# Kernel optimization log

Measured on AMD Instinct MI355X. Metric: run time of the kernel, lower is better.

The kernel has to match this reference:

```python
import jax, jax.numpy as jnp
import numpy as np

NUM_HEADS = 16
SLICE_SIZE = 1024
SCALING = SLICE_SIZE ** 0.5  # module divides by sqrt(slice_size), as written


def setup_inputs() -> dict:
    key = jax.random.key(0)
    ks = jax.random.split(key, 9)
    B, S, D = 4, 2048, SLICE_SIZE
    sc = 0.02
    return {
        "x": jax.random.normal(ks[0], (B, S, D), dtype=jnp.float32),
        "Wq": jax.random.normal(ks[1], (D, D), dtype=jnp.float32) * sc,
        "bq": jax.random.normal(ks[2], (D,), dtype=jnp.float32) * sc,
        "Wk": jax.random.normal(ks[3], (D, D), dtype=jnp.float32) * sc,
        "bk": jax.random.normal(ks[4], (D,), dtype=jnp.float32) * sc,
        "Wv": jax.random.normal(ks[5], (D, D), dtype=jnp.float32) * sc,
        "bv": jax.random.normal(ks[6], (D,), dtype=jnp.float32) * sc,
        "Wp": jax.random.normal(ks[7], (D, D), dtype=jnp.float32) * sc,
        "bp": jax.random.normal(ks[8], (D,), dtype=jnp.float32) * sc,
    }


def _split_heads(t):
    # 'b s (h o) -> b h s o'
    b, s, d = t.shape
    return t.reshape(b, s, NUM_HEADS, d // NUM_HEADS).transpose(0, 2, 1, 3)


def reference(x, Wq, bq, Wk, bk, Wv, bv, Wp, bp):
    q = _split_heads(x @ Wq.T + bq)  # [B,H,S,O]
    k = _split_heads(x @ Wk.T + bk)
    v = _split_heads(x @ Wv.T + bv)
    energy = jnp.einsum('bhqo,bhko->bhqk', q, k)  # full score matrix
    attn = jax.nn.softmax(energy / SCALING, axis=-1)
    # Faithful to source: 'b h q k, b h v o -> b h v o' sums attn over (q,k)
    out = jnp.einsum('bhqk,bhvo->bhvo', attn, v)
    b, h, s, o = out.shape
    out = out.transpose(0, 2, 1, 3).reshape(b, s, h * o)  # 'b h v o -> b v (h o)'
    return out @ Wp.T + bp
```

## Files before the change

kernel.cpp:

```cpp
#include <hip/hip_runtime.h>
#include <cstdint>


typedef unsigned short u16;
typedef __bf16 bf16x8 __attribute__((ext_vector_type(8)));
typedef unsigned short u16x8 __attribute__((ext_vector_type(8)));
typedef float f32x4 __attribute__((ext_vector_type(4)));

__device__ __forceinline__ u16 f2bf(float f) {
  unsigned int u = __float_as_uint(f);
  u += 0x7fffu + ((u >> 16) & 1u);
  return (u16)(u >> 16);
}

__device__ __forceinline__ void load16(const void* g, void* l) {
  auto gp = (const __attribute__((address_space(1))) unsigned int*)(uintptr_t)g;
  auto lp = (__attribute__((address_space(3))) unsigned int*)(unsigned int)(uintptr_t)l;
  __builtin_amdgcn_global_load_lds(gp, lp, 16, 0, 0);
}

__global__ void k_prep(const float* __restrict__ Wv, const float* __restrict__ bv,
                       const float* __restrict__ Wp, const float* __restrict__ bp,
                       u16* __restrict__ wvtb, float* __restrict__ cv) {
  __shared__ float tile[32][33];
  const int b = blockIdx.x;
  const int tid = threadIdx.x;
  if (b < 1024) {
    const int bi = (b & 31) * 32;
    const int bj = (b >> 5) * 32;
    const int tx = tid & 31;
    const int ty = tid >> 5;
    for (int r = ty; r < 32; r += 8)
      tile[r][tx] = Wv[(long)(bj + r) * 1024 + bi + tx];
    __syncthreads();
    for (int r = ty; r < 32; r += 8)
      wvtb[(long)(bi + r) * 1024 + bj + tx] = f2bf(tile[tx][r]);
  } else {
    const int row = (b - 1024) * 4 + (tid >> 6);
    const int lane = tid & 63;
    const float* w = Wp + (long)row * 1024;
    float s = 0.f;
    for (int j = lane; j < 1024; j += 64) s += w[j] * bv[j];
    for (int off = 32; off; off >>= 1) s += __shfl_down(s, off, 64);
    if (lane == 0) cv[row] = 2048.f * s + bp[row];
  }
}

__global__ void k_reduce(const float* __restrict__ p, u16* __restrict__ dst) {
  const long i = (long)(blockIdx.x * 256 + threadIdx.x) * 4;
  const float4 a = *(const float4*)(p + i);
  const float4 b = *(const float4*)(p + 1048576 + i);
  const float4 c = *(const float4*)(p + 2097152 + i);
  const float4 d = *(const float4*)(p + 3145728 + i);
  ushort4 o;
  o.x = f2bf((a.x + b.x + c.x + d.x) * 2048.f);
  o.y = f2bf((a.y + b.y + c.y + d.y) * 2048.f);
  o.z = f2bf((a.z + b.z + c.z + d.z) * 2048.f);
  o.w = f2bf((a.w + b.w + c.w + d.w) * 2048.f);
  *(ushort4*)(dst + i) = o;
}

template <int MODE, int NB>
__global__ __launch_bounds__(256, 3) void k_gemm(
    const float* __restrict__ A, const u16* __restrict__ B, float* __restrict__ Out,
    const float* __restrict__ bias, int M, int N, int K) {
  __shared__ u16 As[64 * 64];
  __shared__ u16 Bs[256 * 64];

  const int tid = threadIdx.x;
  const int lane = tid & 63;
  const int wv = tid >> 6;
  const int waveN = wv << 6;
  const int l15 = lane & 15;
  const int quad = lane >> 4;

  long bm, bn;
  int kBeg, kEnd;
  if constexpr (MODE == 0) {
    const int id = blockIdx.x;
    const int xcd = id & 7;
    const int j = id >> 3;
    const int mPerXcd = M / 64 / 8;
    bm = (long)(xcd * mPerXcd + j / NB) * 64;
    bn = (long)(j % NB) * 256;
    kBeg = 0; kEnd = K;
  } else {
    bm = (long)blockIdx.x * 64;
    bn = (long)blockIdx.y * 256;
    const int kChunk = K / gridDim.z;
    kBeg = blockIdx.z * kChunk;
    kEnd = kBeg + kChunk;
  }

  const int ar = tid >> 2;
  const int acg = tid & 3;
  const float* Ap = A + (bm + ar) * (long)K + acg * 16;
  const int x0 = (acg * 2) ^ (ar & 7);
  u16* Aw0 = As + ar * 64 + x0 * 8;
  u16* Aw1 = As + ar * 64 + (x0 ^ 1) * 8;

  const int srow = tid >> 3;
  const int sslot = tid & 7;

  const f32x4 zero = {0.f, 0.f, 0.f, 0.f};
  f32x4 acc[4][4];
#pragma unroll
  for (int i = 0; i < 4; ++i)
#pragma unroll
    for (int j = 0; j < 4; ++j) acc[i][j] = zero;

  for (int k0 = kBeg; k0 < kEnd; k0 += 64) {
    __syncthreads();
#pragma unroll
    for (int r = 0; r < 8; ++r) {
      const int row = r * 32 + srow;
      const int kc = sslot ^ (row & 7);
      load16(B + (bn + row) * K + k0 + kc * 8, Bs + r * 2048 + wv * 512);
    }
    {
      const float4* ap = (const float4*)(Ap + k0);
      const float4 f0 = ap[0], f1 = ap[1], f2 = ap[2], f3 = ap[3];
      u16x8 c0, c1;
      c0[0] = f2bf(f0.x); c0[1] = f2bf(f0.y); c0[2] = f2bf(f0.z); c0[3] = f2bf(f0.w);
      c0[4] = f2bf(f1.x); c0[5] = f2bf(f1.y); c0[6] = f2bf(f1.z); c0[7] = f2bf(f1.w);
      c1[0] = f2bf(f2.x); c1[1] = f2bf(f2.y); c1[2] = f2bf(f2.z); c1[3] = f2bf(f2.w);
      c1[4] = f2bf(f3.x); c1[5] = f2bf(f3.y); c1[6] = f2bf(f3.z); c1[7] = f2bf(f3.w);
      *(u16x8*)Aw0 = c0;
      *(u16x8*)Aw1 = c1;
    }
    __syncthreads();

#pragma unroll
    for (int h = 0; h < 2; ++h) {
      bf16x8 af[4], bg[4];
#pragma unroll
      for (int t = 0; t < 4; ++t) {
        const int xk = ((h << 2) + quad) ^ (l15 & 7);
        af[t] = *(const bf16x8*)(As + (t * 16 + l15) * 64 + xk * 8);
        bg[t] = *(const bf16x8*)(Bs + (waveN + t * 16 + l15) * 64 + xk * 8);
      }
#pragma unroll
      for (int i = 0; i < 4; ++i)
#pragma unroll
        for (int j = 0; j < 4; ++j)
          acc[i][j] = __builtin_amdgcn_mfma_f32_16x16x32_bf16(af[i], bg[j], acc[i][j], 0, 0, 0);
    }
  }

  float* outp = (MODE == 1) ? Out + (long)blockIdx.z * M * N : Out;
#pragma unroll
  for (int i = 0; i < 4; ++i) {
    const long gm = bm + i * 16 + quad * 4;
#pragma unroll
    for (int j = 0; j < 4; ++j) {
      const long gn = bn + waveN + j * 16 + l15;
      const float bb = (MODE == 0) ? bias[gn] : 0.f;
#pragma unroll
      for (int r = 0; r < 4; ++r)
        outp[(gm + r) * N + gn] = acc[i][j][r] + bb;
    }
  }
}

extern "C" void kernel_launch(void* const* d_in, const int* in_sizes, int n_in,
                              void* d_out, int out_size, void* d_ws, size_t ws_size,
                              hipStream_t stream) {
  const float* x  = (const float*)d_in[0];
  const float* Wv = (const float*)d_in[5];
  const float* bv = (const float*)d_in[6];
  const float* Wp = (const float*)d_in[7];
  const float* bp = (const float*)d_in[8];

  char* ws = (char*)d_ws;
  u16* wvtb  = (u16*)(ws);
  u16* m2b   = (u16*)(ws + (2u << 20));
  float* cv  = (float*)(ws + (4u << 20));
  float* m2f = (float*)(ws + (4u << 20) + 4096);

  k_prep<<<1280, 256, 0, stream>>>(Wv, bv, Wp, bp, wvtb, cv);

  k_gemm<1, 4><<<dim3(16, 4, 4), 256, 0, stream>>>(Wp, wvtb, m2f, nullptr,
                                                   1024, 1024, 1024);
  k_reduce<<<1024, 256, 0, stream>>>(m2f, m2b);

  k_gemm<0, 4><<<512, 256, 0, stream>>>(x, m2b, (float*)d_out, cv,
                                        8192, 1024, 1024);
}
```

Measured before the change: 153.6 us.

## Halve GEMM N-tile to 128 and register-prefetch next A tile

```diff
diff --git a/kernel.cpp b/kernel.cpp
--- a/kernel.cpp
+++ b/kernel.cpp
@@ -60,17 +60,17 @@
   *(ushort4*)(dst + i) = o;
 }
 
-template <int MODE, int NB>
-__global__ __launch_bounds__(256, 3) void k_gemm(
+template <int MODE>
+__global__ __launch_bounds__(256, 4) void k_gemm(
     const float* __restrict__ A, const u16* __restrict__ B, float* __restrict__ Out,
     const float* __restrict__ bias, int M, int N, int K) {
   __shared__ u16 As[64 * 64];
-  __shared__ u16 Bs[256 * 64];
+  __shared__ u16 Bs[128 * 64];
 
   const int tid = threadIdx.x;
   const int lane = tid & 63;
   const int wv = tid >> 6;
-  const int waveN = wv << 6;
+  const int waveN = wv << 5;
   const int l15 = lane & 15;
   const int quad = lane >> 4;
 
@@ -80,13 +80,14 @@
     const int id = blockIdx.x;
     const int xcd = id & 7;
     const int j = id >> 3;
+    const int nb = N >> 7;
     const int mPerXcd = M / 64 / 8;
-    bm = (long)(xcd * mPerXcd + j / NB) * 64;
-    bn = (long)(j % NB) * 256;
+    bm = (long)(xcd * mPerXcd + j / nb) * 64;
+    bn = (long)(j % nb) * 128;
     kBeg = 0; kEnd = K;
   } else {
     bm = (long)blockIdx.x * 64;
-    bn = (long)blockIdx.y * 256;
+    bn = (long)blockIdx.y * 128;
     const int kChunk = K / gridDim.z;
     kBeg = blockIdx.z * kChunk;
     kEnd = kBeg + kChunk;
@@ -103,46 +104,58 @@
   const int sslot = tid & 7;
 
   const f32x4 zero = {0.f, 0.f, 0.f, 0.f};
-  f32x4 acc[4][4];
+  f32x4 acc[4][2];
 #pragma unroll
   for (int i = 0; i < 4; ++i)
 #pragma unroll
-    for (int j = 0; j < 4; ++j) acc[i][j] = zero;
+    for (int j = 0; j < 2; ++j) acc[i][j] = zero;
+
+  float4 Ar0, Ar1, Ar2, Ar3;
+  {
+    const float4* ap = (const float4*)(Ap + kBeg);
+    Ar0 = ap[0]; Ar1 = ap[1]; Ar2 = ap[2]; Ar3 = ap[3];
+  }
 
   for (int k0 = kBeg; k0 < kEnd; k0 += 64) {
     __syncthreads();
 #pragma unroll
-    for (int r = 0; r < 8; ++r) {
+    for (int r = 0; r < 4; ++r) {
       const int row = r * 32 + srow;
       const int kc = sslot ^ (row & 7);
       load16(B + (bn + row) * K + k0 + kc * 8, Bs + r * 2048 + wv * 512);
     }
     {
-      const float4* ap = (const float4*)(Ap + k0);
-      const float4 f0 = ap[0], f1 = ap[1], f2 = ap[2], f3 = ap[3];
       u16x8 c0, c1;
-      c0[0] = f2bf(f0.x); c0[1] = f2bf(f0.y); c0[2] = f2bf(f0.z); c0[3] = f2bf(f0.w);
-      c0[4] = f2bf(f1.x); c0[5] = f2bf(f1.y); c0[6] = f2bf(f1.z); c0[7] = f2bf(f1.w);
-      c1[0] = f2bf(f2.x); c1[1] = f2bf(f2.y); c1[2] = f2bf(f2.z); c1[3] = f2bf(f2.w);
-      c1[4] = f2bf(f3.x); c1[5] = f2bf(f3.y); c1[6] = f2bf(f3.z); c1[7] = f2bf(f3.w);
+      c0[0] = f2bf(Ar0.x); c0[1] = f2bf(Ar0.y); c0[2] = f2bf(Ar0.z); c0[3] = f2bf(Ar0.w);
+      c0[4] = f2bf(Ar1.x); c0[5] = f2bf(Ar1.y); c0[6] = f2bf(Ar1.z); c0[7] = f2bf(Ar1.w);
+      c1[0] = f2bf(Ar2.x); c1[1] = f2bf(Ar2.y); c1[2] = f2bf(Ar2.z); c1[3] = f2bf(Ar2.w);
+      c1[4] = f2bf(Ar3.x); c1[5] = f2bf(Ar3.y); c1[6] = f2bf(Ar3.z); c1[7] = f2bf(Ar3.w);
       *(u16x8*)Aw0 = c0;
       *(u16x8*)Aw1 = c1;
     }
+    if (k0 + 64 < kEnd) {
+      const float4* ap = (const float4*)(Ap + k0 + 64);
+      Ar0 = ap[0]; Ar1 = ap[1]; Ar2 = ap[2]; Ar3 = ap[3];
+    }
     __syncthreads();
 
 #pragma unroll
     for (int h = 0; h < 2; ++h) {
-      bf16x8 af[4], bg[4];
+      bf16x8 af[4], bg[2];
 #pragma unroll
       for (int t = 0; t < 4; ++t) {
         const int xk = ((h << 2) + quad) ^ (l15 & 7);
         af[t] = *(const bf16x8*)(As + (t * 16 + l15) * 64 + xk * 8);
+      }
+#pragma unroll
+      for (int t = 0; t < 2; ++t) {
+        const int xk = ((h << 2) + quad) ^ (l15 & 7);
         bg[t] = *(const bf16x8*)(Bs + (waveN + t * 16 + l15) * 64 + xk * 8);
       }
 #pragma unroll
       for (int i = 0; i < 4; ++i)
 #pragma unroll
-        for (int j = 0; j < 4; ++j)
+        for (int j = 0; j < 2; ++j)
           acc[i][j] = __builtin_amdgcn_mfma_f32_16x16x32_bf16(af[i], bg[j], acc[i][j], 0, 0, 0);
     }
   }
@@ -152,7 +165,7 @@
   for (int i = 0; i < 4; ++i) {
     const long gm = bm + i * 16 + quad * 4;
 #pragma unroll
-    for (int j = 0; j < 4; ++j) {
+    for (int j = 0; j < 2; ++j) {
       const long gn = bn + waveN + j * 16 + l15;
       const float bb = (MODE == 0) ? bias[gn] : 0.f;
 #pragma unroll
@@ -179,10 +192,10 @@
 
   k_prep<<<1280, 256, 0, stream>>>(Wv, bv, Wp, bp, wvtb, cv);
 
-  k_gemm<1, 4><<<dim3(16, 4, 4), 256, 0, stream>>>(Wp, wvtb, m2f, nullptr,
-                                                   1024, 1024, 1024);
+  k_gemm<1><<<dim3(16, 8, 4), 256, 0, stream>>>(Wp, wvtb, m2f, nullptr,
+                                                1024, 1024, 1024);
   k_reduce<<<1024, 256, 0, stream>>>(m2f, m2b);
 
-  k_gemm<0, 4><<<512, 256, 0, stream>>>(x, m2b, (float*)d_out, cv,
-                                        8192, 1024, 1024);
-}
+  k_gemm<0><<<1024, 256, 0, stream>>>(x, m2b, (float*)d_out, cv,
+                                      8192, 1024, 1024);
+}
```

Result: slower. 158.5 us (+3.2%).
